# Optimization experiments

Measured on AMD Instinct MI355X. Metric: run time of the kernel, lower is better.

Reference implementation:

```python
import jax, jax.numpy as jnp
import numpy as np

NH, NKV, HD = 16, 8, 128  # heads, kv heads, head dim
N_REP = NH // NKV
EPS = 1e-06
K_MASK = float(jnp.finfo(jnp.bfloat16).min)
SCALE = HD ** -0.5


def _rms_norm(x, w):
    xf = x.astype(jnp.float32)
    rms = jnp.sqrt(jnp.mean(xf * xf, axis=-1, keepdims=True) + EPS)
    return (xf / rms * w).astype(x.dtype)


def _rotate_half(x):
    x1, x2 = jnp.split(x, 2, axis=-1)
    return jnp.concatenate([-x2, x1], axis=-1)


def setup_inputs() -> dict:
    key = jax.random.key(0)
    ks = jax.random.split(key, 5)
    B, S, H = 1, 2048, 2048
    hidden_states = jax.random.normal(ks[0], (B, S, H), jnp.float32)
    # real RoPE tables (duplicated-half layout), theta = 5e6
    pos = jnp.arange(S, dtype=jnp.float32)
    inv_freq = 1.0 / (5_000_000.0 ** (jnp.arange(0, HD, 2, dtype=jnp.float32) / HD))
    ang = pos[:, None] * inv_freq[None, :]            # (S, HD/2)
    emb = jnp.concatenate([ang, ang], axis=-1)[None]  # (1, S, HD)
    cos, sin = jnp.cos(emb), jnp.sin(emb)
    attention_mask = jnp.tril(jnp.ones((S, S), bool))[None, None]  # causal (1,1,S,S)
    sc = 0.02
    wq = jax.random.normal(ks[1], (H, NH * HD), jnp.float32) * sc
    wk = jax.random.normal(ks[2], (H, NKV * HD), jnp.float32) * sc
    wv = jax.random.normal(ks[3], (H, NKV * HD), jnp.float32) * sc
    wo = jax.random.normal(ks[4], (NH * HD, H), jnp.float32) * sc
    q_norm_w = jnp.ones((HD,), jnp.float32)
    k_norm_w = jnp.ones((HD,), jnp.float32)
    return {"hidden_states": hidden_states, "cos": cos, "sin": sin,
            "attention_mask": attention_mask, "wq": wq, "wk": wk, "wv": wv,
            "wo": wo, "q_norm_w": q_norm_w, "k_norm_w": k_norm_w}


def reference(hidden_states, cos, sin, attention_mask, wq, wk, wv, wo, q_norm_w, k_norm_w):
    B, S, H = hidden_states.shape
    q = (hidden_states @ wq).reshape(B, S, NH, HD)
    k = (hidden_states @ wk).reshape(B, S, NKV, HD)
    v = (hidden_states @ wv).reshape(B, S, NKV, HD)
    q = _rms_norm(q, q_norm_w)
    k = _rms_norm(k, k_norm_w)
    c = cos[:, :, None, :]
    s = sin[:, :, None, :]
    q = q * c + _rotate_half(q) * s
    k = k * c + _rotate_half(k) * s
    # GQA: group q heads by kv head; same math as jnp.repeat + matmul
    qg = q.reshape(B, S, NKV, N_REP, HD)
    scores = jnp.einsum('bqgrd,bkgd->bgrqk', qg, k) * SCALE  # (B,NKV,N_REP,S,S)
    scores = jnp.where(attention_mask[:, :, None], scores, K_MASK)
    attn = jax.nn.softmax(scores.astype(jnp.float32), axis=-1).astype(q.dtype)
    out = jnp.einsum('bgrqk,bkgd->bqgrd', attn, v)            # (B,S,NKV,N_REP,HD)
    out = out.reshape(B, S, NH * HD)
    return out @ wo
```

## Files before the change

### kernel.cpp

```cpp
#include <hip/hip_runtime.h>
#include <hip/hip_bf16.h>
#include <stdint.h>

typedef _Float16 half8 __attribute__((ext_vector_type(8)));
typedef _Float16 half4 __attribute__((ext_vector_type(4)));
typedef float f32x4 __attribute__((ext_vector_type(4)));

#define MFMA16(A, B, C) __builtin_amdgcn_mfma_f32_16x16x32_f16(A, B, C, 0, 0, 0)

static constexpr int Sdim = 2048;
static constexpr int NH = 16;
static constexpr int NKV = 8;
static constexpr int HD = 128;
static constexpr float ATT_SCALE = 0.08838834764831845f;
static constexpr float S0 = 4.0f;

__device__ __forceinline__ void async_copy16(const _Float16* g, _Float16* l) {
  auto gp = reinterpret_cast<const __attribute__((address_space(1))) uint32_t*>(
      reinterpret_cast<uintptr_t>(g));
  auto lp = reinterpret_cast<__attribute__((address_space(3))) uint32_t*>(
      reinterpret_cast<uintptr_t>(l));
  __builtin_amdgcn_global_load_lds(gp, lp, 16, 0, 0);
}

__global__ __launch_bounds__(256) void xconv(const float* __restrict__ X,
                                             _Float16* __restrict__ Xh) {
  int i = (blockIdx.x * 256 + threadIdx.x) * 4;
  float4 v = *(const float4*)(X + i);
  half4 h = {(_Float16)v.x, (_Float16)v.y, (_Float16)v.z, (_Float16)v.w};
  *(half4*)(Xh + i) = h;
}

__global__ __launch_bounds__(256) void wtrans(const float* __restrict__ W,
                                              _Float16* __restrict__ WT,
                                              int K, int N) {
  __shared__ __align__(16) float tile[64][68];
  int n0 = blockIdx.x * 64, k0 = blockIdx.y * 64;
  int t = threadIdx.x;
  int c = (t & 15) * 4;
  int rb = t >> 4;
  for (int p = 0; p < 4; ++p) {
    int k = p * 16 + rb;
    *(float4*)&tile[k][c] = *(const float4*)(W + (size_t)(k0 + k) * N + n0 + c);
  }
  __syncthreads();
  int n = t >> 2;
  int kc = (t & 3) * 16;
  half8 o0, o1;
  for (int i = 0; i < 8; ++i) {
    o0[i] = (_Float16)tile[kc + i][n];
    o1[i] = (_Float16)tile[kc + 8 + i][n];
  }
  _Float16* dst = WT + (size_t)(n0 + n) * K + k0 + kc;
  *(half8*)dst = o0;
  *(half8*)(dst + 8) = o1;
}

template <int NI>
__device__ __forceinline__ void stage64(const _Float16* __restrict__ src, size_t stride,
                                        int k0, _Float16* lds, int w, int lane) {
  for (int ii = 0; ii < NI; ++ii) {
    int i = w * NI + ii;
    int row = i * 8 + (lane >> 3);
    int c = (lane & 7) ^ (row & 7);
    async_copy16(src + (size_t)row * stride + k0 + c * 8, lds + i * 512);
  }
}

__device__ __forceinline__ int frag_off(int row, int ks, int quad, int col) {
  return row * 64 + (((ks << 2) | quad) ^ (col & 7)) * 8;
}

__global__ __launch_bounds__(256) void gemm_qkv(const _Float16* __restrict__ Xh,
                                                const _Float16* __restrict__ wqT,
                                                const _Float16* __restrict__ wkT,
                                                const _Float16* __restrict__ wvT,
                                                _Float16* __restrict__ Q,
                                                _Float16* __restrict__ K,
                                                _Float16* __restrict__ Vt) {
  __shared__ __align__(16) _Float16 As[128 * 64];
  __shared__ __align__(16) _Float16 Bs[128 * 64];
  int bx = blockIdx.x, m0 = blockIdx.y * 128;
  const _Float16* BT;
  _Float16* outp;
  int n0, Nst;
  bool vt;
  if (bx < 16)      { BT = wqT; outp = Q;  n0 = bx * 128;        vt = false; Nst = 2048; }
  else if (bx < 24) { BT = wkT; outp = K;  n0 = (bx - 16) * 128; vt = false; Nst = 1024; }
  else              { BT = wvT; outp = Vt; n0 = (bx - 24) * 128; vt = true;  Nst = 2048; }
  int t = threadIdx.x, lane = t & 63, w = t >> 6;
  int col = lane & 15, quad = lane >> 4;
  int wm = (w & 1) * 64, wn = (w >> 1) * 64;
  f32x4 acc[4][4] = {};
  for (int k0 = 0; k0 < 2048; k0 += 64) {
    stage64<4>(Xh + (size_t)m0 * 2048, 2048, k0, As, w, lane);
    stage64<4>(BT + (size_t)n0 * 2048, 2048, k0, Bs, w, lane);
    __syncthreads();
    half8 af[4][2], bf[4][2];
    for (int i = 0; i < 4; ++i)
      for (int ks = 0; ks < 2; ++ks) {
        af[i][ks] = *(const half8*)(As + frag_off(wm + i * 16 + col, ks, quad, col));
        bf[i][ks] = *(const half8*)(Bs + frag_off(wn + i * 16 + col, ks, quad, col));
      }
    for (int ks = 0; ks < 2; ++ks)
      for (int i = 0; i < 4; ++i)
        for (int j = 0; j < 4; ++j)
          acc[i][j] = MFMA16(af[i][ks], bf[j][ks], acc[i][j]);
    __syncthreads();
  }
  if (!vt) {
    for (int i = 0; i < 4; ++i)
      for (int j = 0; j < 4; ++j)
        for (int r = 0; r < 4; ++r) {
          int m = m0 + wm + i * 16 + quad * 4 + r;
          int n = n0 + wn + j * 16 + col;
          outp[(size_t)m * Nst + n] = (_Float16)acc[i][j][r];
        }
  } else {
    for (int i = 0; i < 4; ++i)
      for (int j = 0; j < 4; ++j) {
        int n = n0 + wn + j * 16 + col;
        int mb = m0 + wm + i * 16 + quad * 4;
        half4 hv = {(_Float16)acc[i][j][0], (_Float16)acc[i][j][1],
                    (_Float16)acc[i][j][2], (_Float16)acc[i][j][3]};
        *(half4*)(outp + (size_t)n * Sdim + mb) = hv;
      }
  }
}

__global__ __launch_bounds__(256) void gemm_o(const _Float16* __restrict__ A,
                                              const _Float16* __restrict__ BT,
                                              float* __restrict__ C) {
  __shared__ __align__(16) _Float16 As[64 * 64];
  __shared__ __align__(16) _Float16 Bs[128 * 64];
  int m0 = blockIdx.y * 64, n0 = blockIdx.x * 128;
  int t = threadIdx.x, lane = t & 63, w = t >> 6;
  int col = lane & 15, quad = lane >> 4;
  int wm = (w & 1) * 32, wn = (w >> 1) * 64;
  f32x4 acc[2][4] = {};
  for (int k0 = 0; k0 < 2048; k0 += 64) {
    stage64<2>(A + (size_t)m0 * 2048, 2048, k0, As, w, lane);
    stage64<4>(BT + (size_t)n0 * 2048, 2048, k0, Bs, w, lane);
    __syncthreads();
    half8 af[2][2], bf[4][2];
    for (int ks = 0; ks < 2; ++ks) {
      for (int i = 0; i < 2; ++i)
        af[i][ks] = *(const half8*)(As + frag_off(wm + i * 16 + col, ks, quad, col));
      for (int j = 0; j < 4; ++j)
        bf[j][ks] = *(const half8*)(Bs + frag_off(wn + j * 16 + col, ks, quad, col));
    }
    for (int ks = 0; ks < 2; ++ks)
      for (int i = 0; i < 2; ++i)
        for (int j = 0; j < 4; ++j)
          acc[i][j] = MFMA16(af[i][ks], bf[j][ks], acc[i][j]);
    __syncthreads();
  }
  for (int i = 0; i < 2; ++i)
    for (int j = 0; j < 4; ++j)
      for (int r = 0; r < 4; ++r) {
        int m = m0 + wm + i * 16 + quad * 4 + r;
        int n = n0 + wn + j * 16 + col;
        C[(size_t)m * 2048 + n] = acc[i][j][r];
      }
}

__global__ __launch_bounds__(256) void rmsrope(const _Float16* __restrict__ src,
                                               _Float16* __restrict__ dst,
                                               const float* __restrict__ cs,
                                               const float* __restrict__ sn,
                                               const float* __restrict__ nw,
                                               int nh, float scale) {
  int w = threadIdx.x >> 6, lane = threadIdx.x & 63;
  int idx = blockIdx.x * 4 + w;
  int m = idx / nh, h = idx - m * nh;
  const _Float16* p = src + (size_t)m * nh * HD + h * HD;
  float x0 = (float)p[lane], x1 = (float)p[lane + 64];
  float ss = x0 * x0 + x1 * x1;
#pragma unroll
  for (int o = 32; o > 0; o >>= 1) ss += __shfl_xor(ss, o);
  float inv = rsqrtf(ss * (1.0f / 128.0f) + 1e-6f);
  float n0v = x0 * inv * nw[lane], n1v = x1 * inv * nw[lane + 64];
  float c0 = cs[m * HD + lane], c1 = cs[m * HD + lane + 64];
  float s0 = sn[m * HD + lane], s1 = sn[m * HD + lane + 64];
  _Float16* q = dst + (size_t)m * nh * HD + h * HD;
  q[lane] = (_Float16)((n0v * c0 - n1v * s0) * scale);
  q[lane + 64] = (_Float16)((n1v * c1 + n0v * s1) * scale);
}

__global__ __launch_bounds__(256) void fattn(const _Float16* __restrict__ Qn,
                                             const _Float16* __restrict__ Kn,
                                             const _Float16* __restrict__ Vt,
                                             _Float16* __restrict__ Op,
                                             float* __restrict__ lp) {
  __shared__ __align__(16) _Float16 Ks[64 * 128];
  __shared__ __align__(16) _Float16 Vs[128 * 64];
  __shared__ __align__(16) _Float16 Ps[4 * 1024];
  int qb = (int)gridDim.x - 1 - (int)blockIdx.x;
  int h = blockIdx.y, g = h >> 1, s = blockIdx.z;
  int t = threadIdx.x, lane = t & 63, w = t >> 6;
  int col = lane & 15, quad = lane >> 4;
  half8 qf[4];
  {
    int qrow = qb * 64 + w * 16 + col;
    for (int kc = 0; kc < 4; ++kc)
      qf[kc] = *(const half8*)(Qn + (size_t)qrow * (NH * HD) + h * HD + kc * 32 + quad * 8);
  }
  _Float16* Psw = Ps + w * 1024;
  f32x4 O[8] = {};
  float li[4] = {0.0f, 0.0f, 0.0f, 0.0f};
  for (int kt = s; kt <= qb; kt += 2) {
    for (int ii = 0; ii < 4; ++ii) {
      int i = w * 4 + ii;
      int krow = i * 4 + (lane >> 4);
      int kc = (lane & 15) ^ (krow & 15);
      async_copy16(Kn + (size_t)(kt * 64 + krow) * (NKV * HD) + g * HD + kc * 8,
                   Ks + i * 512);
      int vrow = i * 8 + (lane >> 3);
      int vc = (lane & 7) ^ (vrow & 7);
      async_copy16(Vt + (size_t)(g * HD + vrow) * Sdim + kt * 64 + vc * 8,
                   Vs + i * 512);
    }
    __syncthreads();
    f32x4 Sc[4];
    for (int nt = 0; nt < 4; ++nt) {
      f32x4 a = {};
      for (int kc = 0; kc < 4; ++kc) {
        half8 b = *(const half8*)(Ks + (nt * 16 + col) * 128 + ((4 * kc + quad) ^ col) * 8);
        a = MFMA16(qf[kc], b, a);
      }
      Sc[nt] = a;
    }
    if (kt == qb) {
      for (int nt = 0; nt < 4; ++nt)
        for (int r = 0; r < 4; ++r)
          if ((nt * 16 + col) > (w * 16 + quad * 4 + r)) Sc[nt][r] = -1e4f;
    }
    for (int nt = 0; nt < 4; ++nt)
      for (int r = 0; r < 4; ++r) {
        float pv = __expf(Sc[nt][r] - S0);
        Sc[nt][r] = pv;
        li[r] += pv;
      }
    for (int nt = 0; nt < 4; ++nt)
      for (int r = 0; r < 4; ++r) {
        int q = quad * 4 + r;
        Psw[q * 64 + (((2 * nt + (col >> 3)) ^ (q & 7)) * 8) + (col & 7)] =
            (_Float16)Sc[nt][r];
      }
    for (int c2 = 0; c2 < 2; ++c2) {
      half8 ap = *(const half8*)(Psw + col * 64 + (((4 * c2 + quad) ^ (col & 7)) * 8));
      for (int nt = 0; nt < 8; ++nt) {
        half8 bv = *(const half8*)(Vs + (nt * 16 + col) * 64 +
                                   (((4 * c2 + quad) ^ (col & 7)) * 8));
        O[nt] = MFMA16(ap, bv, O[nt]);
      }
    }
    __syncthreads();
  }
  for (int r = 0; r < 4; ++r) {
    float sm = li[r];
    sm += __shfl_xor(sm, 1);
    sm += __shfl_xor(sm, 2);
    sm += __shfl_xor(sm, 4);
    sm += __shfl_xor(sm, 8);
    li[r] = sm;
  }
  _Float16* op = Op + (size_t)s * Sdim * (NH * HD);
  for (int nt = 0; nt < 8; ++nt)
    for (int r = 0; r < 4; ++r) {
      int m = qb * 64 + w * 16 + quad * 4 + r;
      op[(size_t)m * (NH * HD) + h * HD + nt * 16 + col] = (_Float16)O[nt][r];
    }
  if (col == 0) {
    float* lpp = lp + (size_t)s * NH * Sdim + (size_t)h * Sdim;
    for (int r = 0; r < 4; ++r) lpp[qb * 64 + w * 16 + quad * 4 + r] = li[r];
  }
}

__global__ __launch_bounds__(256) void merge(const _Float16* __restrict__ Op,
                                             const float* __restrict__ lp,
                                             _Float16* __restrict__ attn) {
  int m = blockIdx.x, t = threadIdx.x;
  int h = t >> 4, d0 = (t & 15) * 8;
  size_t off = (size_t)m * (NH * HD) + h * HD + d0;
  half8 o0 = *(const half8*)(Op + off);
  half8 o1 = *(const half8*)(Op + (size_t)Sdim * NH * HD + off);
  float l = lp[(size_t)h * Sdim + m] + lp[(size_t)NH * Sdim + (size_t)h * Sdim + m];
  float ri = 1.0f / l;
  half8 o;
  for (int i = 0; i < 8; ++i) o[i] = (_Float16)(((float)o0[i] + (float)o1[i]) * ri);
  *(half8*)(attn + off) = o;
}

extern "C" void kernel_launch(void* const* d_in, const int* in_sizes, int n_in,
                              void* d_out, int out_size, void* d_ws, size_t ws_size,
                              hipStream_t stream) {
  (void)in_sizes; (void)n_in; (void)out_size; (void)ws_size;
  const float* X  = (const float*)d_in[0];
  const float* cs = (const float*)d_in[1];
  const float* sn = (const float*)d_in[2];
  const float* wq = (const float*)d_in[4];
  const float* wk = (const float*)d_in[5];
  const float* wv = (const float*)d_in[6];
  const float* wo = (const float*)d_in[7];
  const float* qw = (const float*)d_in[8];
  const float* kw = (const float*)d_in[9];
  char* ws = (char*)d_ws;
  const size_t MB = 1024 * 1024;
  _Float16* wqT  = (_Float16*)(ws + 0 * MB);
  _Float16* wkT  = (_Float16*)(ws + 8 * MB);
  _Float16* wvT  = (_Float16*)(ws + 12 * MB);
  _Float16* woT  = (_Float16*)(ws + 16 * MB);
  _Float16* Xh   = (_Float16*)(ws + 24 * MB);
  _Float16* Qraw = (_Float16*)(ws + 32 * MB);
  _Float16* Kraw = (_Float16*)(ws + 40 * MB);
  _Float16* Vt   = (_Float16*)(ws + 44 * MB);
  _Float16* Qn   = (_Float16*)(ws + 48 * MB);
  _Float16* Kn   = (_Float16*)(ws + 56 * MB);
  float*    lp   = (float*)(ws + 60 * MB);
  _Float16* Op   = wqT;
  _Float16* attn = Qraw;
  float* out = (float*)d_out;

  xconv<<<4096, 256, 0, stream>>>(X, Xh);
  wtrans<<<dim3(32, 32), 256, 0, stream>>>(wq, wqT, 2048, 2048);
  wtrans<<<dim3(16, 32), 256, 0, stream>>>(wk, wkT, 2048, 1024);
  wtrans<<<dim3(16, 32), 256, 0, stream>>>(wv, wvT, 2048, 1024);
  wtrans<<<dim3(32, 32), 256, 0, stream>>>(wo, woT, 2048, 2048);

  gemm_qkv<<<dim3(32, 16), 256, 0, stream>>>(Xh, wqT, wkT, wvT, Qraw, Kraw, Vt);

  rmsrope<<<2048 * 16 / 4, 256, 0, stream>>>(Qraw, Qn, cs, sn, qw, 16, ATT_SCALE);
  rmsrope<<<2048 * 8 / 4, 256, 0, stream>>>(Kraw, Kn, cs, sn, kw, 8, 1.0f);

  fattn<<<dim3(32, 16, 2), 256, 0, stream>>>(Qn, Kn, Vt, Op, lp);
  merge<<<2048, 256, 0, stream>>>(Op, lp, attn);

  gemm_o<<<dim3(16, 32), 256, 0, stream>>>(attn, woT, out);
}
```

Before: 284.8 us.

## Merge launches, vectorize GEMM epilogues via swapped MFMA, split attention KV three ways

New measurement: 269.7 us. -5.3%, faster.

```diff
diff --git a/kernel.cpp b/kernel.cpp
--- a/kernel.cpp
+++ b/kernel.cpp
@@ -31,9 +31,25 @@
   *(half4*)(Xh + i) = h;
 }
 
-__global__ __launch_bounds__(256) void wtrans(const float* __restrict__ W,
-                                              _Float16* __restrict__ WT,
-                                              int K, int N) {
+__global__ __launch_bounds__(256) void wtrans_all(const float* __restrict__ wq,
+                                                  const float* __restrict__ wk,
+                                                  const float* __restrict__ wv,
+                                                  const float* __restrict__ wo,
+                                                  _Float16* __restrict__ wqT,
+                                                  _Float16* __restrict__ wkT,
+                                                  _Float16* __restrict__ wvT,
+                                                  _Float16* __restrict__ woT) {
+  const float* W;
+  _Float16* WT;
+  int N;
+  switch (blockIdx.z) {
+    case 0: W = wq; WT = wqT; N = 2048; break;
+    case 1: W = wk; WT = wkT; N = 1024; break;
+    case 2: W = wv; WT = wvT; N = 1024; break;
+    default: W = wo; WT = woT; N = 2048; break;
+  }
+  if ((int)blockIdx.x * 64 >= N) return;
+  const int K = 2048;
   __shared__ __align__(16) float tile[64][68];
   int n0 = blockIdx.x * 64, k0 = blockIdx.y * 64;
   int t = threadIdx.x;
@@ -102,20 +118,28 @@
         af[i][ks] = *(const half8*)(As + frag_off(wm + i * 16 + col, ks, quad, col));
         bf[i][ks] = *(const half8*)(Bs + frag_off(wn + i * 16 + col, ks, quad, col));
       }
-    for (int ks = 0; ks < 2; ++ks)
-      for (int i = 0; i < 4; ++i)
-        for (int j = 0; j < 4; ++j)
-          acc[i][j] = MFMA16(af[i][ks], bf[j][ks], acc[i][j]);
+    if (!vt) {
+      for (int ks = 0; ks < 2; ++ks)
+        for (int i = 0; i < 4; ++i)
+          for (int j = 0; j < 4; ++j)
+            acc[i][j] = MFMA16(bf[j][ks], af[i][ks], acc[i][j]);
+    } else {
+      for (int ks = 0; ks < 2; ++ks)
+        for (int i = 0; i < 4; ++i)
+          for (int j = 0; j < 4; ++j)
+            acc[i][j] = MFMA16(af[i][ks], bf[j][ks], acc[i][j]);
+    }
     __syncthreads();
   }
   if (!vt) {
     for (int i = 0; i < 4; ++i)
-      for (int j = 0; j < 4; ++j)
-        for (int r = 0; r < 4; ++r) {
-          int m = m0 + wm + i * 16 + quad * 4 + r;
-          int n = n0 + wn + j * 16 + col;
-          outp[(size_t)m * Nst + n] = (_Float16)acc[i][j][r];
-        }
+      for (int j = 0; j < 4; ++j) {
+        int m = m0 + wm + i * 16 + col;
+        int n = n0 + wn + j * 16 + quad * 4;
+        half4 hv = {(_Float16)acc[i][j][0], (_Float16)acc[i][j][1],
+                    (_Float16)acc[i][j][2], (_Float16)acc[i][j][3]};
+        *(half4*)(outp + (size_t)m * Nst + n) = hv;
+      }
   } else {
     for (int i = 0; i < 4; ++i)
       for (int j = 0; j < 4; ++j) {
@@ -152,27 +176,38 @@
     for (int ks = 0; ks < 2; ++ks)
       for (int i = 0; i < 2; ++i)
         for (int j = 0; j < 4; ++j)
-          acc[i][j] = MFMA16(af[i][ks], bf[j][ks], acc[i][j]);
+          acc[i][j] = MFMA16(bf[j][ks], af[i][ks], acc[i][j]);
     __syncthreads();
   }
   for (int i = 0; i < 2; ++i)
-    for (int j = 0; j < 4; ++j)
-      for (int r = 0; r < 4; ++r) {
-        int m = m0 + wm + i * 16 + quad * 4 + r;
-        int n = n0 + wn + j * 16 + col;
-        C[(size_t)m * 2048 + n] = acc[i][j][r];
-      }
-}
-
-__global__ __launch_bounds__(256) void rmsrope(const _Float16* __restrict__ src,
-                                               _Float16* __restrict__ dst,
-                                               const float* __restrict__ cs,
-                                               const float* __restrict__ sn,
-                                               const float* __restrict__ nw,
-                                               int nh, float scale) {
+    for (int j = 0; j < 4; ++j) {
+      int m = m0 + wm + i * 16 + col;
+      int n = n0 + wn + j * 16 + quad * 4;
+      *(f32x4*)(C + (size_t)m * 2048 + n) = acc[i][j];
+    }
+}
+
+__global__ __launch_bounds__(256) void rmsrope_all(const _Float16* __restrict__ Qraw,
+                                                   const _Float16* __restrict__ Kraw,
+                                                   _Float16* __restrict__ Qn,
+                                                   _Float16* __restrict__ Kn,
+                                                   const float* __restrict__ cs,
+                                                   const float* __restrict__ sn,
+                                                   const float* __restrict__ qw,
+                                                   const float* __restrict__ kw) {
   int w = threadIdx.x >> 6, lane = threadIdx.x & 63;
-  int idx = blockIdx.x * 4 + w;
-  int m = idx / nh, h = idx - m * nh;
+  int gw = blockIdx.x * 4 + w;
+  const _Float16* src;
+  _Float16* dst;
+  const float* nw;
+  int m, h, nh;
+  float scale;
+  if (gw < Sdim * NH) {
+    m = gw >> 4; h = gw & 15; nh = NH; src = Qraw; dst = Qn; nw = qw; scale = ATT_SCALE;
+  } else {
+    int g2 = gw - Sdim * NH;
+    m = g2 >> 3; h = g2 & 7; nh = NKV; src = Kraw; dst = Kn; nw = kw; scale = 1.0f;
+  }
   const _Float16* p = src + (size_t)m * nh * HD + h * HD;
   float x0 = (float)p[lane], x1 = (float)p[lane + 64];
   float ss = x0 * x0 + x1 * x1;
@@ -190,7 +225,8 @@
 __global__ __launch_bounds__(256) void fattn(const _Float16* __restrict__ Qn,
                                              const _Float16* __restrict__ Kn,
                                              const _Float16* __restrict__ Vt,
-                                             _Float16* __restrict__ Op,
+                                             _Float16* __restrict__ Op01,
+                                             _Float16* __restrict__ Op2,
                                              float* __restrict__ lp) {
   __shared__ __align__(16) _Float16 Ks[64 * 128];
   __shared__ __align__(16) _Float16 Vs[128 * 64];
@@ -208,7 +244,7 @@
   _Float16* Psw = Ps + w * 1024;
   f32x4 O[8] = {};
   float li[4] = {0.0f, 0.0f, 0.0f, 0.0f};
-  for (int kt = s; kt <= qb; kt += 2) {
+  for (int kt = s; kt <= qb; kt += 3) {
     for (int ii = 0; ii < 4; ++ii) {
       int i = w * 4 + ii;
       int krow = i * 4 + (lane >> 4);
@@ -265,7 +301,7 @@
     sm += __shfl_xor(sm, 8);
     li[r] = sm;
   }
-  _Float16* op = Op + (size_t)s * Sdim * (NH * HD);
+  _Float16* op = (s == 2) ? Op2 : Op01 + (size_t)s * Sdim * (NH * HD);
   for (int nt = 0; nt < 8; ++nt)
     for (int r = 0; r < 4; ++r) {
       int m = qb * 64 + w * 16 + quad * 4 + r;
@@ -277,18 +313,23 @@
   }
 }
 
-__global__ __launch_bounds__(256) void merge(const _Float16* __restrict__ Op,
+__global__ __launch_bounds__(256) void merge(const _Float16* __restrict__ Op01,
+                                             const _Float16* __restrict__ Op2,
                                              const float* __restrict__ lp,
                                              _Float16* __restrict__ attn) {
   int m = blockIdx.x, t = threadIdx.x;
   int h = t >> 4, d0 = (t & 15) * 8;
   size_t off = (size_t)m * (NH * HD) + h * HD + d0;
-  half8 o0 = *(const half8*)(Op + off);
-  half8 o1 = *(const half8*)(Op + (size_t)Sdim * NH * HD + off);
-  float l = lp[(size_t)h * Sdim + m] + lp[(size_t)NH * Sdim + (size_t)h * Sdim + m];
+  half8 o0 = *(const half8*)(Op01 + off);
+  half8 o1 = *(const half8*)(Op01 + (size_t)Sdim * NH * HD + off);
+  half8 o2 = *(const half8*)(Op2 + off);
+  float l = lp[(size_t)h * Sdim + m] +
+            lp[(size_t)NH * Sdim + (size_t)h * Sdim + m] +
+            lp[2 * (size_t)NH * Sdim + (size_t)h * Sdim + m];
   float ri = 1.0f / l;
   half8 o;
-  for (int i = 0; i < 8; ++i) o[i] = (_Float16)(((float)o0[i] + (float)o1[i]) * ri);
+  for (int i = 0; i < 8; ++i)
+    o[i] = (_Float16)(((float)o0[i] + (float)o1[i] + (float)o2[i]) * ri);
   *(half8*)(attn + off) = o;
 }
 
@@ -318,23 +359,21 @@
   _Float16* Qn   = (_Float16*)(ws + 48 * MB);
   _Float16* Kn   = (_Float16*)(ws + 56 * MB);
   float*    lp   = (float*)(ws + 60 * MB);
-  _Float16* Op   = wqT;
+  _Float16* Op01 = wqT;
+  _Float16* Op2  = Xh;
   _Float16* attn = Qraw;
   float* out = (float*)d_out;
 
   xconv<<<4096, 256, 0, stream>>>(X, Xh);
-  wtrans<<<dim3(32, 32), 256, 0, stream>>>(wq, wqT, 2048, 2048);
-  wtrans<<<dim3(16, 32), 256, 0, stream>>>(wk, wkT, 2048, 1024);
-  wtrans<<<dim3(16, 32), 256, 0, stream>>>(wv, wvT, 2048, 1024);
-  wtrans<<<dim3(32, 32), 256, 0, stream>>>(wo, woT, 2048, 2048);
+  wtrans_all<<<dim3(32, 32, 4), 256, 0, stream>>>(wq, wk, wv, wo, wqT, wkT, wvT, woT);
 
   gemm_qkv<<<dim3(32, 16), 256, 0, stream>>>(Xh, wqT, wkT, wvT, Qraw, Kraw, Vt);
 
-  rmsrope<<<2048 * 16 / 4, 256, 0, stream>>>(Qraw, Qn, cs, sn, qw, 16, ATT_SCALE);
-  rmsrope<<<2048 * 8 / 4, 256, 0, stream>>>(Kraw, Kn, cs, sn, kw, 8, 1.0f);
-
-  fattn<<<dim3(32, 16, 2), 256, 0, stream>>>(Qn, Kn, Vt, Op, lp);
-  merge<<<2048, 256, 0, stream>>>(Op, lp, attn);
+  rmsrope_all<<<(Sdim * NH + Sdim * NKV) / 4, 256, 0, stream>>>(Qraw, Kraw, Qn, Kn,
+                                                                cs, sn, qw, kw);
+
+  fattn<<<dim3(32, 16, 3), 256, 0, stream>>>(Qn, Kn, Vt, Op01, Op2, lp);
+  merge<<<2048, 256, 0, stream>>>(Op01, Op2, lp, attn);
 
   gemm_o<<<dim3(16, 32), 256, 0, stream>>>(attn, woT, out);
 }
```
